# Optimization experiments

Measured on AMD Instinct MI355X. Metric: run time of the kernel, lower is better.

The kernel has to match this reference:

```python
import jax, jax.numpy as jnp
import numpy as np

N = 100000      # total nodes
E = 800000      # directed edges
DIN = 256       # input feature dim
H = 128         # hidden dim
EPS = 1e-5      # BatchNorm eps


def setup_inputs() -> dict:
    key = jax.random.key(0)
    ks = jax.random.split(key, 18)
    s = 0.05
    return {
        "x": jax.random.normal(ks[0], (N, DIN), jnp.float32),
        "src": jax.random.randint(ks[1], (E,), 0, N, dtype=jnp.int32),
        "dst": jax.random.randint(ks[2], (E,), 0, N, dtype=jnp.int32),
        "W1": jax.random.normal(ks[3], (DIN, H), jnp.float32) * s,
        "b1": jnp.zeros((H,), jnp.float32),
        "g1": jnp.ones((H,), jnp.float32),
        "be1": jnp.zeros((H,), jnp.float32),
        "W2": jax.random.normal(ks[4], (H, H), jnp.float32) * s,
        "b2": jnp.zeros((H,), jnp.float32),
        "g2": jnp.ones((H,), jnp.float32),
        "be2": jnp.zeros((H,), jnp.float32),
        "W3": jax.random.normal(ks[5], (H, H), jnp.float32) * s,
        "b3": jnp.zeros((H,), jnp.float32),
        "g3": jnp.ones((H,), jnp.float32),
        "be3": jnp.zeros((H,), jnp.float32),
        "Wf": jax.random.normal(ks[6], (H, 1), jnp.float32) * s,
        "bf": jnp.zeros((1,), jnp.float32),
    }


def _gcn_conv(h, W, b, src, dst, dis):
    # GCNConv: project, then sym-normalized aggregation over edges + self-loops
    h = h @ W                                   # [N, out]
    coef = dis[src] * dis[dst]                  # [E] edge norm weights
    agg = jax.ops.segment_sum(h[src] * coef[:, None], dst, num_segments=N)
    agg = agg + h * (dis * dis)[:, None]        # self-loop term (norm = 1/deg)
    return agg + b


def _bn_relu(h, g, be):
    # BatchNorm1d in training mode (batch stats over nodes, biased variance)
    mu = jnp.mean(h, axis=0)
    var = jnp.var(h, axis=0)
    return jax.nn.relu((h - mu) * (g / jnp.sqrt(var + EPS)) + be)


def reference(x, src, dst, W1, b1, g1, be1, W2, b2, g2, be2,
              W3, b3, g3, be3, Wf, bf):
    # degree of (A + I) counted on destination nodes, edge weight 1
    deg = jax.ops.segment_sum(jnp.ones((E,), jnp.float32), dst, num_segments=N) + 1.0
    dis = jax.lax.rsqrt(deg)                    # deg >= 1, safe

    h = _bn_relu(_gcn_conv(x, W1, b1, src, dst, dis), g1, be1)
    h = _bn_relu(_gcn_conv(h, W2, b2, src, dst, dis), g2, be2)
    h = _bn_relu(_gcn_conv(h, W3, b3, src, dst, dis), g3, be3)
    return h @ Wf + bf                          # [N, 1]
```

## Files before the change

### kernel.cpp

```cpp
#include <hip/hip_runtime.h>
#include <hip/hip_bf16.h>

typedef unsigned short ushort_t;
typedef __bf16 bf16x8 __attribute__((ext_vector_type(8)));
typedef unsigned short ushort8 __attribute__((ext_vector_type(8)));
typedef unsigned short ushort4v __attribute__((ext_vector_type(4)));
typedef float f32x4 __attribute__((ext_vector_type(4)));

#define HH 128
#define EPS 1e-5f
#define STAT_SLICES 32
#define MTILE 32
#define GAS __attribute__((address_space(1)))
#define LAS __attribute__((address_space(3)))

__device__ __forceinline__ float bf2f(ushort_t u) {
    unsigned v = ((unsigned)u) << 16;
    return __builtin_bit_cast(float, v);
}
__device__ __forceinline__ ushort_t f2bf(float f) {
    unsigned u = __builtin_bit_cast(unsigned, f);
    unsigned r = (u + 0x7fffu + ((u >> 16) & 1u)) >> 16;
    return (ushort_t)r;
}
__device__ __forceinline__ float cvt(const void* p, int i, int flag) {
    return flag ? bf2f(((const ushort_t*)p)[i]) : ((const float*)p)[i];
}
__device__ __forceinline__ void dma16(const void* g, void* l) {
    __builtin_amdgcn_global_load_lds((const GAS unsigned*)g, (LAS unsigned*)l, 16, 0, 0);
}
__device__ __forceinline__ void acc8(const uint4 w, float c, float a[8]) {
    unsigned x0 = w.x, x1 = w.y, x2 = w.z, x3 = w.w;
    a[0] = fmaf(__builtin_bit_cast(float, x0 << 16), c, a[0]);
    a[1] = fmaf(__builtin_bit_cast(float, x0 & 0xffff0000u), c, a[1]);
    a[2] = fmaf(__builtin_bit_cast(float, x1 << 16), c, a[2]);
    a[3] = fmaf(__builtin_bit_cast(float, x1 & 0xffff0000u), c, a[3]);
    a[4] = fmaf(__builtin_bit_cast(float, x2 << 16), c, a[4]);
    a[5] = fmaf(__builtin_bit_cast(float, x2 & 0xffff0000u), c, a[5]);
    a[6] = fmaf(__builtin_bit_cast(float, x3 << 16), c, a[6]);
    a[7] = fmaf(__builtin_bit_cast(float, x3 & 0xffff0000u), c, a[7]);
}

__global__ void preK(const int* __restrict__ dst, int* __restrict__ counts, int E,
                     const void* W1, ushort_t* Wt1, const void* W2, ushort_t* Wt2,
                     const void* W3, ushort_t* Wt3,
                     const void* g1, const void* b1, const void* b2, const void* b3,
                     const void* g2, const void* g3, const void* be1, const void* be2,
                     const void* be3, const void* Wfp, const void* bfp,
                     float* __restrict__ cvec, int histB) {
    const int bid = blockIdx.x;
    const int tid = threadIdx.x;
    const int flag = (((const ushort_t*)g1)[0] == 0x3F80) ? 1 : 0;
    if (bid < histB) {
        int e = bid * 256 + tid;
        if (e < E) atomicAdd(&counts[dst[e]], 1);
    } else if (bid < histB + 256) {
        int idx = (bid - histB) * 256 + tid;
        const void* W; ushort_t* Wt; int K;
        if (idx < 32768)      { W = W1; Wt = Wt1; K = 256; }
        else if (idx < 49152) { W = W2; Wt = Wt2; K = 128; idx -= 32768; }
        else                  { W = W3; Wt = Wt3; K = 128; idx -= 49152; }
        int k = idx >> 7, nn = idx & 127;
        Wt[nn * K + k] = flag ? ((const ushort_t*)W)[idx] : f2bf(((const float*)W)[idx]);
    } else {
        int t = tid;
        if (t < 128) {
            cvec[t]        = cvt(b1, t, flag);
            cvec[128 + t]  = cvt(b2, t, flag);
            cvec[256 + t]  = cvt(b3, t, flag);
            cvec[384 + t]  = cvt(g1, t, flag);
            cvec[512 + t]  = cvt(g2, t, flag);
            cvec[640 + t]  = cvt(g3, t, flag);
            cvec[768 + t]  = cvt(be1, t, flag);
            cvec[896 + t]  = cvt(be2, t, flag);
            cvec[1024 + t] = cvt(be3, t, flag);
            cvec[1152 + t] = cvt(Wfp, t, flag);
            if (t == 0) cvec[1280] = cvt(bfp, 0, flag);
        }
    }
}

__global__ void scanAdisK(const int* __restrict__ cnt, int* __restrict__ partial,
                          float* __restrict__ dis, int n, int nbScan) {
    __shared__ int lds[256];
    const int tid = threadIdx.x;
    if ((int)blockIdx.x < nbScan) {
        int base = blockIdx.x * 2048 + tid * 8;
        int s = 0;
#pragma unroll
        for (int j = 0; j < 8; ++j) { int idx = base + j; if (idx < n) s += cnt[idx]; }
        lds[tid] = s; __syncthreads();
        for (int off = 128; off; off >>= 1) { if (tid < off) lds[tid] += lds[tid + off]; __syncthreads(); }
        if (tid == 0) partial[blockIdx.x] = lds[0];
    } else {
        int i = (blockIdx.x - nbScan) * 256 + tid;
        if (i < n) dis[i] = rsqrtf((float)cnt[i] + 1.0f);
    }
}

__device__ __forceinline__ void scanC2Dev(int* lds, const int* __restrict__ cnt,
                                          const int* __restrict__ partial,
                                          int* __restrict__ rowptr, int n, int bid, int nb) {
    const int tid = threadIdx.x;
    int pre = 0, tot = 0;
    for (int i = 0; i < nb; ++i) { int v = partial[i]; if (i < bid) pre += v; tot += v; }
    int base = bid * 2048 + tid * 8;
    int v[8]; int s = 0;
#pragma unroll
    for (int j = 0; j < 8; ++j) { int idx = base + j; v[j] = (idx < n) ? cnt[idx] : 0; s += v[j]; }
    lds[tid] = s; __syncthreads();
    for (int off = 1; off < 256; off <<= 1) {
        int x = (tid >= off) ? lds[tid - off] : 0;
        __syncthreads();
        lds[tid] += x;
        __syncthreads();
    }
    int excl = lds[tid] - s;
    int off0 = pre + excl;
#pragma unroll
    for (int j = 0; j < 8; ++j) {
        int idx = base + j;
        if (idx < n) { rowptr[idx] = off0; off0 += v[j]; }
    }
    if (bid == 0 && tid == 0) rowptr[n] = tot;
}

__global__ void scatterK(const int* __restrict__ src, const int* __restrict__ dst,
                         const int* __restrict__ rowptr, int* __restrict__ fill,
                         const float* __restrict__ dis,
                         uint2* __restrict__ erec, int E) {
    int e = blockIdx.x * 256 + threadIdx.x;
    if (e >= E) return;
    int d = dst[e], s = src[e];
    int old = atomicSub(&fill[d], 1);
    int pos = rowptr[d] + old - 1;
    float c = dis[s] * dis[d];
    uint2 r; r.x = (unsigned)s; r.y = __builtin_bit_cast(unsigned, c);
    erec[pos] = r;
}

__global__ __launch_bounds__(256) void mm1scanCK(const void* __restrict__ x,
                                                 const ushort_t* __restrict__ Wt1,
                                                 ushort_t* __restrict__ tbuf, int n,
                                                 const ushort_t* __restrict__ flagRef,
                                                 const int* __restrict__ cnt,
                                                 const int* __restrict__ partial,
                                                 int* __restrict__ rowptr, int nbScan) {
    __shared__ char smem[33792];
    const int tid = threadIdx.x;
    if ((int)blockIdx.x < nbScan) {
        scanC2Dev((int*)smem, cnt, partial, rowptr, n, blockIdx.x, nbScan);
        return;
    }
    const int arm = blockIdx.x - nbScan;
    const int NB  = gridDim.x - nbScan;
    const int nTiles = (n + MTILE - 1) / MTILE;
    if (arm >= nTiles) return;

    const int lane = tid & 63, wave = tid >> 6;
    const int m = lane & 15, q = lane >> 4;
    const int flag = (flagRef[0] == 0x3F80) ? 1 : 0;

    ushort8 wfrag[8][2];
#pragma unroll
    for (int s = 0; s < 8; ++s)
#pragma unroll
        for (int tt = 0; tt < 2; ++tt)
            wfrag[s][tt] = *(const ushort8*)&Wt1[(size_t)((wave * 2 + tt) * 16 + m) * 256 + s * 32 + q * 8];

    const int sr = tid >> 3, sa = tid & 7;
    char* buf0 = smem;
    char* buf1 = smem + 16384;

    float4  f[8];
    ushort8 v[4];

    auto stageLoad = [&](int T) {
        int row = T * MTILE + sr; if (row >= n) row = n - 1;
        if (flag) {
            const ushort_t* xp = (const ushort_t*)x + (size_t)row * 256 + sa * 32;
#pragma unroll
            for (int j = 0; j < 4; ++j) v[j] = *(const ushort8*)(xp + j * 8);
        } else {
            const float* xp = (const float*)x + (size_t)row * 256 + sa * 32;
#pragma unroll
            for (int j = 0; j < 8; ++j) f[j] = *(const float4*)(xp + j * 4);
        }
    };
    auto convWrite = [&](char* buf) {
        if (!flag) {
#pragma unroll
            for (int j = 0; j < 4; ++j) {
                float4 a = f[2 * j], b = f[2 * j + 1];
                ushort8 t8;
                t8[0] = f2bf(a.x); t8[1] = f2bf(a.y); t8[2] = f2bf(a.z); t8[3] = f2bf(a.w);
                t8[4] = f2bf(b.x); t8[5] = f2bf(b.y); t8[6] = f2bf(b.z); t8[7] = f2bf(b.w);
                v[j] = t8;
            }
        }
#pragma unroll
        for (int j = 0; j < 4; ++j) {
            int u = (sa * 4 + j) ^ (sr & 7);
            *(ushort8*)(buf + sr * 512 + u * 16) = v[j];
        }
    };
    auto computeStore = [&](int T, const char* buf) {
        f32x4 acc[2][2];
#pragma unroll
        for (int bb = 0; bb < 2; ++bb)
#pragma unroll
            for (int tt = 0; tt < 2; ++tt) acc[bb][tt] = (f32x4){0.f, 0.f, 0.f, 0.f};
#pragma unroll
        for (int bb = 0; bb < 2; ++bb) {
            const char* base = buf + (bb * 16 + m) * 512;
#pragma unroll
            for (int s = 0; s < 8; ++s) {
                ushort8 xf = *(const ushort8*)(base + (((s * 4 + q) ^ (m & 7)) * 16));
                bf16x8 xb = __builtin_bit_cast(bf16x8, xf);
#pragma unroll
                for (int tt = 0; tt < 2; ++tt)
                    acc[bb][tt] = __builtin_amdgcn_mfma_f32_16x16x32_bf16(
                        __builtin_bit_cast(bf16x8, wfrag[s][tt]), xb, acc[bb][tt], 0, 0, 0);
            }
        }
#pragma unroll
        for (int bb = 0; bb < 2; ++bb) {
            int node = T * MTILE + bb * 16 + m;
            if (node < n) {
#pragma unroll
                for (int tt = 0; tt < 2; ++tt) {
                    ushort4v pk;
#pragma unroll
                    for (int r = 0; r < 4; ++r) pk[r] = f2bf(acc[bb][tt][r]);
                    *(ushort4v*)(tbuf + (size_t)node * HH + (wave * 2 + tt) * 16 + q * 4) = pk;
                }
            }
        }
    };

    stageLoad(arm); convWrite(buf0);
    __syncthreads();
    int T = arm, pp = 0;
    while (true) {
        int Tn = T + NB;
        bool more = (Tn < nTiles);
        if (more) stageLoad(Tn);
        computeStore(T, pp ? buf1 : buf0);
        if (!more) break;
        convWrite(pp ? buf0 : buf1);
        __syncthreads();
        T = Tn; pp ^= 1;
    }
}

__global__ __launch_bounds__(256) void mmBNK(const ushort_t* __restrict__ A,
                                             const ushort_t* __restrict__ Wt,
                                             ushort_t* __restrict__ out, int n,
                                             const float* __restrict__ ssum,
                                             const float* __restrict__ ssq,
                                             const float* __restrict__ gam,
                                             const float* __restrict__ bet) {
    __shared__ char smem[50176];
    char* abuf = smem + 32768;
    float* scw = (float*)(smem + 49152);
    const int tid = threadIdx.x;

    if (tid < 128) {
        float S = 0.f, Q = 0.f;
#pragma unroll
        for (int sl = 0; sl < STAT_SLICES; ++sl) { S += ssum[sl * HH + tid]; Q += ssq[sl * HH + tid]; }
        float invn = 1.0f / (float)n;
        float mu = S * invn;
        float var = fmaxf(Q * invn - mu * mu, 0.f);
        float sc = gam[tid] * rsqrtf(var + EPS);
        scw[tid] = sc;
        scw[128 + tid] = bet[tid] - mu * sc;
    }
#pragma unroll
    for (int it = 0; it < 8; ++it) {
        int idx = tid + it * 256;
        int r = idx >> 4, seg = idx & 15;
        int p = seg ^ (r & 7);
        *(uint4*)&smem[r * 256 + p * 16] = *(const uint4*)&Wt[(size_t)r * 128 + seg * 8];
    }
    __syncthreads();

    const int lane = tid & 63, wave = tid >> 6;
    const int m = lane & 15, q = lane >> 4;
    const int nTiles = (n + 63) >> 6;

    for (int tile = blockIdx.x; tile < nTiles; tile += gridDim.x) {
        const int row0 = tile * 64 + wave * 16;
#pragma unroll
        for (int j = 0; j < 4; ++j) {
            int r = row0 + j * 4;
            if (r + 3 >= n) r = n - 4;
            const char* g = (const char*)A + (size_t)r * 256 + lane * 16;
            dma16(g, abuf + (wave * 16 + j * 4) * 256);
        }
        __builtin_amdgcn_s_waitcnt(0x0F70);

        f32x4 acc[8];
#pragma unroll
        for (int t = 0; t < 8; ++t) acc[t] = (f32x4){0.f, 0.f, 0.f, 0.f};
        const char* arow = abuf + (wave * 16 + m) * 256;
#pragma unroll
        for (int s = 0; s < 4; ++s) {
            ushort8 av = *(const ushort8*)(arow + s * 64 + q * 16);
            int kb = s * 32 + q * 8;
#pragma unroll
            for (int j = 0; j < 8; ++j)
                av[j] = f2bf(fmaxf(bf2f(av[j]) * scw[kb + j] + scw[128 + kb + j], 0.f));
            bf16x8 nf = __builtin_bit_cast(bf16x8, av);
#pragma unroll
            for (int t = 0; t < 8; ++t) {
                int p = (s * 4 + q) ^ (m & 7);
                ushort8 wv = *(const ushort8*)&smem[(t * 16 + m) * 256 + p * 16];
                acc[t] = __builtin_amdgcn_mfma_f32_16x16x32_bf16(
                    __builtin_bit_cast(bf16x8, wv), nf, acc[t], 0, 0, 0);
            }
        }
        int node = tile * 64 + wave * 16 + m;
        if (node < n) {
            ushort_t* op = out + (size_t)node * HH + q * 4;
#pragma unroll
            for (int t = 0; t < 8; ++t) {
                ushort4v pk;
#pragma unroll
                for (int r = 0; r < 4; ++r) pk[r] = f2bf(acc[t][r]);
                *(ushort4v*)(op + t * 16) = pk;
            }
        }
    }
}

__global__ __launch_bounds__(256) void aggK(const ushort_t* __restrict__ t,
                                            const uint2* __restrict__ erec,
                                            const int* __restrict__ rowptr,
                                            const float* __restrict__ dis,
                                            const float* __restrict__ bias,
                                            ushort_t* __restrict__ g,
                                            float* __restrict__ ssum, float* __restrict__ ssq,
                                            int n) {
    const int tid  = threadIdx.x;
    const int lane = tid & 63;
    const int wave = tid >> 6;
    const int grp  = lane >> 4;
    const int p    = lane & 15;
    const int cb   = p * 8;

    float bch[8];
#pragma unroll
    for (int j = 0; j < 8; ++j) bch[j] = bias[cb + j];

    float s[8], q[8];
#pragma unroll
    for (int j = 0; j < 8; ++j) { s[j] = 0.f; q[j] = 0.f; }

    for (int node = blockIdx.x * 16 + wave * 4 + grp; node < n; node += gridDim.x * 16) {
        float d = dis[node];
        float d2 = d * d;
        float a[8];
#pragma unroll
        for (int j = 0; j < 8; ++j) a[j] = 0.f;
        uint4 sv = *(const uint4*)(t + (size_t)node * HH + cb);
        acc8(sv, d2, a);

        const int beg = rowptr[node], end = rowptr[node + 1];
        int e = beg;
        for (; e + 8 <= end; e += 8) {
            uint2 rr[8];
#pragma unroll
            for (int kk = 0; kk < 8; ++kk) rr[kk] = erec[e + kk];
            uint4 w0[4];
#pragma unroll
            for (int kk = 0; kk < 4; ++kk)
                w0[kk] = *(const uint4*)(t + (size_t)rr[kk].x * HH + cb);
            uint4 w1[4];
#pragma unroll
            for (int kk = 0; kk < 4; ++kk)
                w1[kk] = *(const uint4*)(t + (size_t)rr[4 + kk].x * HH + cb);
#pragma unroll
            for (int kk = 0; kk < 4; ++kk)
                acc8(w0[kk], __builtin_bit_cast(float, rr[kk].y), a);
#pragma unroll
            for (int kk = 0; kk < 4; ++kk)
                acc8(w1[kk], __builtin_bit_cast(float, rr[4 + kk].y), a);
        }
        if (e < end) {
            uint2 rr[8];
#pragma unroll
            for (int kk = 0; kk < 8; ++kk) {
                int idx = e + kk;
                rr[kk] = (idx < end) ? erec[idx] : (uint2){0u, 0u};
            }
            uint4 w0[4];
#pragma unroll
            for (int kk = 0; kk < 4; ++kk)
                w0[kk] = *(const uint4*)(t + (size_t)rr[kk].x * HH + cb);
            uint4 w1[4];
#pragma unroll
            for (int kk = 0; kk < 4; ++kk)
                w1[kk] = *(const uint4*)(t + (size_t)rr[4 + kk].x * HH + cb);
#pragma unroll
            for (int kk = 0; kk < 4; ++kk)
                acc8(w0[kk], __builtin_bit_cast(float, rr[kk].y), a);
#pragma unroll
            for (int kk = 0; kk < 4; ++kk)
                acc8(w1[kk], __builtin_bit_cast(float, rr[4 + kk].y), a);
        }

        ushort8 pk;
#pragma unroll
        for (int j = 0; j < 8; ++j) {
            a[j] += bch[j];
            pk[j] = f2bf(a[j]);
            s[j] += a[j]; q[j] += a[j] * a[j];
        }
        *(ushort8*)(g + (size_t)node * HH + cb) = pk;
    }

#pragma unroll
    for (int j = 0; j < 8; ++j) {
        s[j] += __shfl_xor(s[j], 16); s[j] += __shfl_xor(s[j], 32);
        q[j] += __shfl_xor(q[j], 16); q[j] += __shfl_xor(q[j], 32);
    }
    __shared__ float red[4][16][16];
    if (grp == 0) {
#pragma unroll
        for (int j = 0; j < 8; ++j) { red[wave][p][j] = s[j]; red[wave][p][8 + j] = q[j]; }
    }
    __syncthreads();
    {
        int ch = tid & 127, kind = tid >> 7;
        float S = 0.f;
#pragma unroll
        for (int w = 0; w < 4; ++w) S += red[w][ch >> 3][kind * 8 + (ch & 7)];
        int slice = (blockIdx.x & (STAT_SLICES - 1)) * HH;
        atomicAdd((kind ? ssq : ssum) + slice + ch, S);
    }
}

__global__ __launch_bounds__(256) void outK(const ushort_t* __restrict__ g,
                                            const float* __restrict__ ssum,
                                            const float* __restrict__ ssq,
                                            const float* __restrict__ gam,
                                            const float* __restrict__ bet,
                                            const float* __restrict__ Wf,
                                            const float* __restrict__ bfp,
                                            void* __restrict__ outv, int n,
                                            const ushort_t* __restrict__ flagRef) {
    __shared__ float scw[256];
    const int tid = threadIdx.x;
    if (tid < 128) {
        float S = 0.f, Q = 0.f;
#pragma unroll
        for (int sl = 0; sl < STAT_SLICES; ++sl) { S += ssum[sl * HH + tid]; Q += ssq[sl * HH + tid]; }
        float invn = 1.0f / (float)n;
        float mu = S * invn;
        float var = fmaxf(Q * invn - mu * mu, 0.f);
        float sc = gam[tid] * rsqrtf(var + EPS);
        scw[tid] = sc;
        scw[128 + tid] = bet[tid] - mu * sc;
    }
    __syncthreads();

    const int lane = tid & 63;
    const int wave = tid >> 6;
    const int grp  = lane >> 4;
    const int p    = lane & 15;
    const int cb   = p * 8;
    float w8[8], sc8[8], sh8[8];
#pragma unroll
    for (int j = 0; j < 8; ++j) {
        w8[j] = Wf[cb + j]; sc8[j] = scw[cb + j]; sh8[j] = scw[128 + cb + j];
    }
    const float bb = bfp[0];
    const int flag = (flagRef[0] == 0x3F80) ? 1 : 0;

    for (int node = blockIdx.x * 16 + wave * 4 + grp; node < n; node += gridDim.x * 16) {
        uint4 v = *(const uint4*)(g + (size_t)node * HH + cb);
        unsigned u[4] = {v.x, v.y, v.z, v.w};
        float x = 0.f;
#pragma unroll
        for (int j = 0; j < 4; ++j) {
            float f0 = __builtin_bit_cast(float, u[j] << 16);
            float f1 = __builtin_bit_cast(float, u[j] & 0xffff0000u);
            x += fmaxf(f0 * sc8[2 * j] + sh8[2 * j], 0.f) * w8[2 * j];
            x += fmaxf(f1 * sc8[2 * j + 1] + sh8[2 * j + 1], 0.f) * w8[2 * j + 1];
        }
#pragma unroll
        for (int off = 8; off; off >>= 1) x += __shfl_xor(x, off);
        if (p == 0) {
            float r = x + bb;
            if (flag) ((ushort_t*)outv)[node] = f2bf(r);
            else      ((float*)outv)[node] = r;
        }
    }
}

extern "C" void kernel_launch(void* const* d_in, const int* in_sizes, int n_in,
                              void* d_out, int out_size, void* d_ws, size_t ws_size,
                              hipStream_t stream) {
    const int DIN = 256;
    const int N = in_sizes[0] / DIN;
    const int E = in_sizes[1];

    const void* x   = d_in[0];
    const int*  src = (const int*)d_in[1];
    const int*  dst = (const int*)d_in[2];
    const void* W1  = d_in[3];
    const void* b1  = d_in[4];
    const void* g1  = d_in[5];
    const void* be1 = d_in[6];
    const void* W2  = d_in[7];
    const void* b2  = d_in[8];
    const void* g2  = d_in[9];
    const void* be2 = d_in[10];
    const void* W3  = d_in[11];
    const void* b3  = d_in[12];
    const void* g3  = d_in[13];
    const void* be3 = d_in[14];
    const void* Wf  = d_in[15];
    const void* bfp = d_in[16];
    const ushort_t* flagRef = (const ushort_t*)g1;

    char* base = (char*)d_ws;
    size_t off = 0;
    auto carve = [&](size_t bytes) -> void* {
        void* p = base + off;
        off += (bytes + 255) & ~(size_t)255;
        return p;
    };
    int*      counts = (int*)carve((size_t)N * 4);
    float*    stats  = (float*)carve((size_t)3 * 2 * STAT_SLICES * HH * 4);
    size_t    zbytes = off;
    float*    dis    = (float*)carve((size_t)N * 4);
    int*      rowptr = (int*)carve((size_t)(N + 1) * 4);
    int*      partial= (int*)carve(256 * 4);
    uint2*    erec   = (uint2*)carve((size_t)E * 8);
    ushort_t* Wt1    = (ushort_t*)carve((size_t)128 * 256 * 2);
    ushort_t* Wt2    = (ushort_t*)carve((size_t)128 * 128 * 2);
    ushort_t* Wt3    = (ushort_t*)carve((size_t)128 * 128 * 2);
    ushort_t* tbuf   = (ushort_t*)carve((size_t)N * HH * 2);
    ushort_t* gbuf   = (ushort_t*)carve((size_t)N * HH * 2);
    float*    cvec   = (float*)carve((size_t)1281 * 4);

    float* ssum0 = stats;                         float* ssq0 = ssum0 + STAT_SLICES * HH;
    float* ssum1 = ssq0 + STAT_SLICES * HH;       float* ssq1 = ssum1 + STAT_SLICES * HH;
    float* ssum2 = ssq1 + STAT_SLICES * HH;       float* ssq2 = ssum2 + STAT_SLICES * HH;

    float* c_b1 = cvec;         float* c_b2 = cvec + 128;  float* c_b3 = cvec + 256;
    float* c_g1 = cvec + 384;   float* c_g2 = cvec + 512;  float* c_g3 = cvec + 640;
    float* c_be1 = cvec + 768;  float* c_be2 = cvec + 896; float* c_be3 = cvec + 1024;
    float* c_Wf = cvec + 1152;  float* c_bf = cvec + 1280;

    const int nbScan = (N + 2047) / 2048;
    const int histB  = (E + 255) / 256;
    const int disB   = (N + 255) / 256;
    const int aggB   = 2048;
    const int mm1B   = 1024;

    hipMemsetAsync(d_ws, 0, zbytes, stream);

    preK<<<histB + 256 + 1, 256, 0, stream>>>(dst, counts, E, W1, Wt1, W2, Wt2, W3, Wt3,
                                              g1, b1, b2, b3, g2, g3, be1, be2, be3, Wf, bfp,
                                              cvec, histB);
    scanAdisK<<<nbScan + disB, 256, 0, stream>>>(counts, partial, dis, N, nbScan);
    mm1scanCK<<<nbScan + mm1B, 256, 0, stream>>>(x, Wt1, tbuf, N, flagRef,
                                                 counts, partial, rowptr, nbScan);
    scatterK<<<histB, 256, 0, stream>>>(src, dst, rowptr, counts, dis, erec, E);

    aggK<<<aggB, 256, 0, stream>>>(tbuf, erec, rowptr, dis, c_b1, gbuf, ssum0, ssq0, N);
    mmBNK<<<768, 256, 0, stream>>>(gbuf, Wt2, tbuf, N, ssum0, ssq0, c_g1, c_be1);
    aggK<<<aggB, 256, 0, stream>>>(tbuf, erec, rowptr, dis, c_b2, gbuf, ssum1, ssq1, N);
    mmBNK<<<768, 256, 0, stream>>>(gbuf, Wt3, tbuf, N, ssum1, ssq1, c_g2, c_be2);
    aggK<<<aggB, 256, 0, stream>>>(tbuf, erec, rowptr, dis, c_b3, gbuf, ssum2, ssq2, N);
    outK<<<1024, 256, 0, stream>>>(gbuf, ssum2, ssq2, c_g3, c_be3, c_Wf, c_bf, d_out, N, flagRef);
}
```

Before: 420.5 us.

## Fuse scatter, aggregation, matmul and output stages into one persistent kernel with grid barriers

Replaces the six kernel launches after the first matmul (scatter, three aggregations, two BN+matmul, output) with one persistent kernel of 1024 blocks that uses a software grid barrier (atomic counter plus release flag) between phases. The matmul phase is also restructured: weight fragments are held in registers, A tiles of 32 rows are double-buffered through LDS with swizzle, and the async LDS DMA path is dropped. This removes launch gaps and per-kernel ramp-up and tail costs. The risks are lower parallelism in the aggregation phases (1024 blocks instead of 2048), spin-wait cost at each barrier, and deadlock if the 1024 blocks cannot all be resident at once.

Result: slower. 1.182 ms (+181.0%).

```diff
diff --git a/kernel.cpp b/kernel.cpp
--- a/kernel.cpp
+++ b/kernel.cpp
@@ -11,8 +11,7 @@
 #define EPS 1e-5f
 #define STAT_SLICES 32
 #define MTILE 32
-#define GAS __attribute__((address_space(1)))
-#define LAS __attribute__((address_space(3)))
+#define FB 1024
 
 __device__ __forceinline__ float bf2f(ushort_t u) {
     unsigned v = ((unsigned)u) << 16;
@@ -25,9 +24,6 @@
 }
 __device__ __forceinline__ float cvt(const void* p, int i, int flag) {
     return flag ? bf2f(((const ushort_t*)p)[i]) : ((const float*)p)[i];
-}
-__device__ __forceinline__ void dma16(const void* g, void* l) {
-    __builtin_amdgcn_global_load_lds((const GAS unsigned*)g, (LAS unsigned*)l, 16, 0, 0);
 }
 __device__ __forceinline__ void acc8(const uint4 w, float c, float a[8]) {
     unsigned x0 = w.x, x1 = w.y, x2 = w.z, x3 = w.w;
@@ -39,6 +35,21 @@
     a[5] = fmaf(__builtin_bit_cast(float, x2 & 0xffff0000u), c, a[5]);
     a[6] = fmaf(__builtin_bit_cast(float, x3 << 16), c, a[6]);
     a[7] = fmaf(__builtin_bit_cast(float, x3 & 0xffff0000u), c, a[7]);
+}
+
+__device__ __forceinline__ void gridSync(int* cnt, int* rel, int phase, int nb) {
+    __syncthreads();
+    if (threadIdx.x == 0) {
+        __threadfence();
+        int prev = atomicAdd(cnt, 1);
+        if (prev == nb * phase - 1) {
+            atomicExch(rel, phase);
+        } else {
+            while (atomicAdd(rel, 0) < phase) __builtin_amdgcn_s_sleep(8);
+        }
+        __threadfence();
+    }
+    __syncthreads();
 }
 
 __global__ void preK(const int* __restrict__ dst, int* __restrict__ counts, int E,
@@ -125,20 +136,6 @@
     if (bid == 0 && tid == 0) rowptr[n] = tot;
 }
 
-__global__ void scatterK(const int* __restrict__ src, const int* __restrict__ dst,
-                         const int* __restrict__ rowptr, int* __restrict__ fill,
-                         const float* __restrict__ dis,
-                         uint2* __restrict__ erec, int E) {
-    int e = blockIdx.x * 256 + threadIdx.x;
-    if (e >= E) return;
-    int d = dst[e], s = src[e];
-    int old = atomicSub(&fill[d], 1);
-    int pos = rowptr[d] + old - 1;
-    float c = dis[s] * dis[d];
-    uint2 r; r.x = (unsigned)s; r.y = __builtin_bit_cast(unsigned, c);
-    erec[pos] = r;
-}
-
 __global__ __launch_bounds__(256) void mm1scanCK(const void* __restrict__ x,
                                                  const ushort_t* __restrict__ Wt1,
                                                  ushort_t* __restrict__ tbuf, int n,
@@ -253,248 +250,286 @@
     }
 }
 
-__global__ __launch_bounds__(256) void mmBNK(const ushort_t* __restrict__ A,
-                                             const ushort_t* __restrict__ Wt,
-                                             ushort_t* __restrict__ out, int n,
-                                             const float* __restrict__ ssum,
-                                             const float* __restrict__ ssq,
-                                             const float* __restrict__ gam,
-                                             const float* __restrict__ bet) {
-    __shared__ char smem[50176];
-    char* abuf = smem + 32768;
-    float* scw = (float*)(smem + 49152);
+__global__ __launch_bounds__(256, 4) void fusedK(
+        const int* __restrict__ src, const int* __restrict__ dst,
+        const int* __restrict__ rowptr, int* __restrict__ fill,
+        const float* __restrict__ dis, uint2* __restrict__ erec, int E,
+        const ushort_t* __restrict__ Wt2, const ushort_t* __restrict__ Wt3,
+        ushort_t* __restrict__ tbuf, ushort_t* __restrict__ gbuf,
+        const float* __restrict__ cvec, float* __restrict__ stats,
+        void* __restrict__ outv, int n, const ushort_t* __restrict__ flagRef,
+        int* __restrict__ bcnt, int* __restrict__ brel) {
+    __shared__ char smem[17408];
+    const int NB  = gridDim.x;
     const int tid = threadIdx.x;
-
-    if (tid < 128) {
-        float S = 0.f, Q = 0.f;
-#pragma unroll
-        for (int sl = 0; sl < STAT_SLICES; ++sl) { S += ssum[sl * HH + tid]; Q += ssq[sl * HH + tid]; }
-        float invn = 1.0f / (float)n;
-        float mu = S * invn;
-        float var = fmaxf(Q * invn - mu * mu, 0.f);
-        float sc = gam[tid] * rsqrtf(var + EPS);
-        scw[tid] = sc;
-        scw[128 + tid] = bet[tid] - mu * sc;
-    }
-#pragma unroll
-    for (int it = 0; it < 8; ++it) {
-        int idx = tid + it * 256;
-        int r = idx >> 4, seg = idx & 15;
-        int p = seg ^ (r & 7);
-        *(uint4*)&smem[r * 256 + p * 16] = *(const uint4*)&Wt[(size_t)r * 128 + seg * 8];
-    }
-    __syncthreads();
-
     const int lane = tid & 63, wave = tid >> 6;
-    const int m = lane & 15, q = lane >> 4;
-    const int nTiles = (n + 63) >> 6;
-
-    for (int tile = blockIdx.x; tile < nTiles; tile += gridDim.x) {
-        const int row0 = tile * 64 + wave * 16;
-#pragma unroll
-        for (int j = 0; j < 4; ++j) {
-            int r = row0 + j * 4;
-            if (r + 3 >= n) r = n - 4;
-            const char* g = (const char*)A + (size_t)r * 256 + lane * 16;
-            dma16(g, abuf + (wave * 16 + j * 4) * 256);
-        }
-        __builtin_amdgcn_s_waitcnt(0x0F70);
-
-        f32x4 acc[8];
-#pragma unroll
-        for (int t = 0; t < 8; ++t) acc[t] = (f32x4){0.f, 0.f, 0.f, 0.f};
-        const char* arow = abuf + (wave * 16 + m) * 256;
-#pragma unroll
-        for (int s = 0; s < 4; ++s) {
-            ushort8 av = *(const ushort8*)(arow + s * 64 + q * 16);
-            int kb = s * 32 + q * 8;
-#pragma unroll
-            for (int j = 0; j < 8; ++j)
-                av[j] = f2bf(fmaxf(bf2f(av[j]) * scw[kb + j] + scw[128 + kb + j], 0.f));
-            bf16x8 nf = __builtin_bit_cast(bf16x8, av);
-#pragma unroll
-            for (int t = 0; t < 8; ++t) {
-                int p = (s * 4 + q) ^ (m & 7);
-                ushort8 wv = *(const ushort8*)&smem[(t * 16 + m) * 256 + p * 16];
-                acc[t] = __builtin_amdgcn_mfma_f32_16x16x32_bf16(
-                    __builtin_bit_cast(bf16x8, wv), nf, acc[t], 0, 0, 0);
-            }
-        }
-        int node = tile * 64 + wave * 16 + m;
-        if (node < n) {
-            ushort_t* op = out + (size_t)node * HH + q * 4;
-#pragma unroll
-            for (int t = 0; t < 8; ++t) {
-                ushort4v pk;
-#pragma unroll
-                for (int r = 0; r < 4; ++r) pk[r] = f2bf(acc[t][r]);
-                *(ushort4v*)(op + t * 16) = pk;
-            }
-        }
-    }
-}
-
-__global__ __launch_bounds__(256) void aggK(const ushort_t* __restrict__ t,
-                                            const uint2* __restrict__ erec,
-                                            const int* __restrict__ rowptr,
-                                            const float* __restrict__ dis,
-                                            const float* __restrict__ bias,
-                                            ushort_t* __restrict__ g,
-                                            float* __restrict__ ssum, float* __restrict__ ssq,
-                                            int n) {
-    const int tid  = threadIdx.x;
-    const int lane = tid & 63;
-    const int wave = tid >> 6;
-    const int grp  = lane >> 4;
-    const int p    = lane & 15;
-    const int cb   = p * 8;
-
-    float bch[8];
-#pragma unroll
-    for (int j = 0; j < 8; ++j) bch[j] = bias[cb + j];
-
-    float s[8], q[8];
-#pragma unroll
-    for (int j = 0; j < 8; ++j) { s[j] = 0.f; q[j] = 0.f; }
-
-    for (int node = blockIdx.x * 16 + wave * 4 + grp; node < n; node += gridDim.x * 16) {
-        float d = dis[node];
-        float d2 = d * d;
-        float a[8];
-#pragma unroll
-        for (int j = 0; j < 8; ++j) a[j] = 0.f;
-        uint4 sv = *(const uint4*)(t + (size_t)node * HH + cb);
-        acc8(sv, d2, a);
-
-        const int beg = rowptr[node], end = rowptr[node + 1];
-        int e = beg;
-        for (; e + 8 <= end; e += 8) {
-            uint2 rr[8];
-#pragma unroll
-            for (int kk = 0; kk < 8; ++kk) rr[kk] = erec[e + kk];
-            uint4 w0[4];
-#pragma unroll
-            for (int kk = 0; kk < 4; ++kk)
-                w0[kk] = *(const uint4*)(t + (size_t)rr[kk].x * HH + cb);
-            uint4 w1[4];
-#pragma unroll
-            for (int kk = 0; kk < 4; ++kk)
-                w1[kk] = *(const uint4*)(t + (size_t)rr[4 + kk].x * HH + cb);
-#pragma unroll
-            for (int kk = 0; kk < 4; ++kk)
-                acc8(w0[kk], __builtin_bit_cast(float, rr[kk].y), a);
-#pragma unroll
-            for (int kk = 0; kk < 4; ++kk)
-                acc8(w1[kk], __builtin_bit_cast(float, rr[4 + kk].y), a);
-        }
-        if (e < end) {
-            uint2 rr[8];
-#pragma unroll
-            for (int kk = 0; kk < 8; ++kk) {
-                int idx = e + kk;
-                rr[kk] = (idx < end) ? erec[idx] : (uint2){0u, 0u};
-            }
-            uint4 w0[4];
-#pragma unroll
-            for (int kk = 0; kk < 4; ++kk)
-                w0[kk] = *(const uint4*)(t + (size_t)rr[kk].x * HH + cb);
-            uint4 w1[4];
-#pragma unroll
-            for (int kk = 0; kk < 4; ++kk)
-                w1[kk] = *(const uint4*)(t + (size_t)rr[4 + kk].x * HH + cb);
-#pragma unroll
-            for (int kk = 0; kk < 4; ++kk)
-                acc8(w0[kk], __builtin_bit_cast(float, rr[kk].y), a);
-#pragma unroll
-            for (int kk = 0; kk < 4; ++kk)
-                acc8(w1[kk], __builtin_bit_cast(float, rr[4 + kk].y), a);
-        }
-
-        ushort8 pk;
+
+    const float* c_b1  = cvec;        const float* c_b2  = cvec + 128;
+    const float* c_b3  = cvec + 256;  const float* c_g1  = cvec + 384;
+    const float* c_g2  = cvec + 512;  const float* c_g3  = cvec + 640;
+    const float* c_be1 = cvec + 768;  const float* c_be2 = cvec + 896;
+    const float* c_be3 = cvec + 1024; const float* c_Wf  = cvec + 1152;
+    const float* c_bf  = cvec + 1280;
+    float* ssum0 = stats;            float* ssq0 = stats + 4096;
+    float* ssum1 = stats + 8192;     float* ssq1 = stats + 12288;
+    float* ssum2 = stats + 16384;    float* ssq2 = stats + 20480;
+
+    for (int e = blockIdx.x * 256 + tid; e < E; e += NB * 256) {
+        int d = dst[e], s = src[e];
+        int old = atomicSub(&fill[d], 1);
+        int pos = rowptr[d] + old - 1;
+        float c = dis[s] * dis[d];
+        uint2 r; r.x = (unsigned)s; r.y = __builtin_bit_cast(unsigned, c);
+        erec[pos] = r;
+    }
+
+    auto aggPhase = [&](const ushort_t* __restrict__ t, ushort_t* __restrict__ g,
+                        const float* __restrict__ bias,
+                        float* __restrict__ ssum, float* __restrict__ ssq) {
+        const int grp = lane >> 4, p = lane & 15, cb = p * 8;
+        float bch[8];
+#pragma unroll
+        for (int j = 0; j < 8; ++j) bch[j] = bias[cb + j];
+        float s[8], q[8];
+#pragma unroll
+        for (int j = 0; j < 8; ++j) { s[j] = 0.f; q[j] = 0.f; }
+
+        for (int node = blockIdx.x * 16 + wave * 4 + grp; node < n; node += NB * 16) {
+            float d = dis[node];
+            float d2 = d * d;
+            float a[8];
+#pragma unroll
+            for (int j = 0; j < 8; ++j) a[j] = 0.f;
+            uint4 sv = *(const uint4*)(t + (size_t)node * HH + cb);
+            acc8(sv, d2, a);
+
+            const int beg = rowptr[node], end = rowptr[node + 1];
+            int e = beg;
+            for (; e + 8 <= end; e += 8) {
+                uint2 rr[8];
+#pragma unroll
+                for (int kk = 0; kk < 8; ++kk) rr[kk] = erec[e + kk];
+                uint4 w0[4];
+#pragma unroll
+                for (int kk = 0; kk < 4; ++kk)
+                    w0[kk] = *(const uint4*)(t + (size_t)rr[kk].x * HH + cb);
+                uint4 w1[4];
+#pragma unroll
+                for (int kk = 0; kk < 4; ++kk)
+                    w1[kk] = *(const uint4*)(t + (size_t)rr[4 + kk].x * HH + cb);
+#pragma unroll
+                for (int kk = 0; kk < 4; ++kk)
+                    acc8(w0[kk], __builtin_bit_cast(float, rr[kk].y), a);
+#pragma unroll
+                for (int kk = 0; kk < 4; ++kk)
+                    acc8(w1[kk], __builtin_bit_cast(float, rr[4 + kk].y), a);
+            }
+            if (e < end) {
+                uint2 rr[8];
+#pragma unroll
+                for (int kk = 0; kk < 8; ++kk) {
+                    int idx = e + kk;
+                    rr[kk] = (idx < end) ? erec[idx] : (uint2){0u, 0u};
+                }
+                uint4 w0[4];
+#pragma unroll
+                for (int kk = 0; kk < 4; ++kk)
+                    w0[kk] = *(const uint4*)(t + (size_t)rr[kk].x * HH + cb);
+                uint4 w1[4];
+#pragma unroll
+                for (int kk = 0; kk < 4; ++kk)
+                    w1[kk] = *(const uint4*)(t + (size_t)rr[4 + kk].x * HH + cb);
+#pragma unroll
+                for (int kk = 0; kk < 4; ++kk)
+                    acc8(w0[kk], __builtin_bit_cast(float, rr[kk].y), a);
+#pragma unroll
+                for (int kk = 0; kk < 4; ++kk)
+                    acc8(w1[kk], __builtin_bit_cast(float, rr[4 + kk].y), a);
+            }
+
+            ushort8 pk;
+#pragma unroll
+            for (int j = 0; j < 8; ++j) {
+                a[j] += bch[j];
+                pk[j] = f2bf(a[j]);
+                s[j] += a[j]; q[j] += a[j] * a[j];
+            }
+            *(ushort8*)(g + (size_t)node * HH + cb) = pk;
+        }
+
 #pragma unroll
         for (int j = 0; j < 8; ++j) {
-            a[j] += bch[j];
-            pk[j] = f2bf(a[j]);
-            s[j] += a[j]; q[j] += a[j] * a[j];
-        }
-        *(ushort8*)(g + (size_t)node * HH + cb) = pk;
-    }
-
-#pragma unroll
-    for (int j = 0; j < 8; ++j) {
-        s[j] += __shfl_xor(s[j], 16); s[j] += __shfl_xor(s[j], 32);
-        q[j] += __shfl_xor(q[j], 16); q[j] += __shfl_xor(q[j], 32);
-    }
-    __shared__ float red[4][16][16];
-    if (grp == 0) {
-#pragma unroll
-        for (int j = 0; j < 8; ++j) { red[wave][p][j] = s[j]; red[wave][p][8 + j] = q[j]; }
-    }
-    __syncthreads();
+            s[j] += __shfl_xor(s[j], 16); s[j] += __shfl_xor(s[j], 32);
+            q[j] += __shfl_xor(q[j], 16); q[j] += __shfl_xor(q[j], 32);
+        }
+        float (*red)[16][16] = (float (*)[16][16])smem;
+        __syncthreads();
+        if (grp == 0) {
+#pragma unroll
+            for (int j = 0; j < 8; ++j) { red[wave][p][j] = s[j]; red[wave][p][8 + j] = q[j]; }
+        }
+        __syncthreads();
+        {
+            int ch = tid & 127, kind = tid >> 7;
+            float S = 0.f;
+#pragma unroll
+            for (int w = 0; w < 4; ++w) S += red[w][ch >> 3][kind * 8 + (ch & 7)];
+            int slice = (blockIdx.x & (STAT_SLICES - 1)) * HH;
+            atomicAdd((kind ? ssq : ssum) + slice + ch, S);
+        }
+    };
+
+    auto mmPhase = [&](const ushort_t* __restrict__ A, const ushort_t* __restrict__ Wt,
+                       ushort_t* __restrict__ out,
+                       const float* __restrict__ ssum, const float* __restrict__ ssq,
+                       const float* __restrict__ gam, const float* __restrict__ bet) {
+        float* scw = (float*)(smem + 16384);
+        if (tid < 128) {
+            float S = 0.f, Q = 0.f;
+#pragma unroll
+            for (int sl = 0; sl < STAT_SLICES; ++sl) { S += ssum[sl * HH + tid]; Q += ssq[sl * HH + tid]; }
+            float invn = 1.0f / (float)n;
+            float mu = S * invn;
+            float var = fmaxf(Q * invn - mu * mu, 0.f);
+            float sc = gam[tid] * rsqrtf(var + EPS);
+            scw[tid] = sc;
+            scw[128 + tid] = bet[tid] - mu * sc;
+        }
+        const int m = lane & 15, q4 = lane >> 4;
+        ushort8 wfrag[4][2];
+#pragma unroll
+        for (int s = 0; s < 4; ++s)
+#pragma unroll
+            for (int tt = 0; tt < 2; ++tt)
+                wfrag[s][tt] = *(const ushort8*)&Wt[(size_t)((wave * 2 + tt) * 16 + m) * 128 + s * 32 + q4 * 8];
+
+        const int sr = tid >> 3, sa = tid & 7;
+        char* b0 = smem;
+        char* b1 = smem + 8192;
+        ushort8 sv[2];
+
+        auto sLoad = [&](int T) {
+            int row = T * 32 + sr; if (row >= n) row = n - 1;
+            const ushort_t* ap = A + (size_t)row * HH + sa * 16;
+            sv[0] = *(const ushort8*)ap;
+            sv[1] = *(const ushort8*)(ap + 8);
+        };
+        auto sWrite = [&](char* buf) {
+#pragma unroll
+            for (int j = 0; j < 2; ++j) {
+                int u = (sa * 2 + j) ^ (sr & 7);
+                *(ushort8*)(buf + sr * 256 + u * 16) = sv[j];
+            }
+        };
+        auto comp = [&](int T, const char* buf) {
+            f32x4 acc[2][2];
+#pragma unroll
+            for (int bb = 0; bb < 2; ++bb)
+#pragma unroll
+                for (int tt = 0; tt < 2; ++tt) acc[bb][tt] = (f32x4){0.f, 0.f, 0.f, 0.f};
+#pragma unroll
+            for (int bb = 0; bb < 2; ++bb) {
+                const char* arow = buf + (bb * 16 + m) * 256;
+#pragma unroll
+                for (int s = 0; s < 4; ++s) {
+                    ushort8 av = *(const ushort8*)(arow + (((s * 4 + q4) ^ (m & 7)) * 16));
+                    int kb = s * 32 + q4 * 8;
+#pragma unroll
+                    for (int j = 0; j < 8; ++j)
+                        av[j] = f2bf(fmaxf(bf2f(av[j]) * scw[kb + j] + scw[128 + kb + j], 0.f));
+                    bf16x8 nf = __builtin_bit_cast(bf16x8, av);
+#pragma unroll
+                    for (int tt = 0; tt < 2; ++tt)
+                        acc[bb][tt] = __builtin_amdgcn_mfma_f32_16x16x32_bf16(
+                            __builtin_bit_cast(bf16x8, wfrag[s][tt]), nf, acc[bb][tt], 0, 0, 0);
+                }
+            }
+#pragma unroll
+            for (int bb = 0; bb < 2; ++bb) {
+                int node = T * 32 + bb * 16 + m;
+                if (node < n) {
+#pragma unroll
+                    for (int tt = 0; tt < 2; ++tt) {
+                        ushort4v pk;
+#pragma unroll
+                        for (int r = 0; r < 4; ++r) pk[r] = f2bf(acc[bb][tt][r]);
+                        *(ushort4v*)(out + (size_t)node * HH + (wave * 2 + tt) * 16 + q4 * 4) = pk;
+                    }
+                }
+            }
+        };
+
+        const int nT = (n + 31) >> 5;
+        int T = blockIdx.x, pp = 0;
+        if (T < nT) sLoad(T);
+        __syncthreads();
+        if (T < nT) sWrite(b0);
+        __syncthreads();
+        while (T < nT) {
+            int Tn = T + NB;
+            if (Tn < nT) sLoad(Tn);
+            comp(T, pp ? b1 : b0);
+            if (Tn >= nT) break;
+            sWrite(pp ? b0 : b1);
+            __syncthreads();
+            T = Tn; pp ^= 1;
+        }
+    };
+
+    gridSync(bcnt, brel, 1, NB);
+    aggPhase(tbuf, gbuf, c_b1, ssum0, ssq0);
+    gridSync(bcnt, brel, 2, NB);
+    mmPhase(gbuf, Wt2, tbuf, ssum0, ssq0, c_g1, c_be1);
+    gridSync(bcnt, brel, 3, NB);
+    aggPhase(tbuf, gbuf, c_b2, ssum1, ssq1);
+    gridSync(bcnt, brel, 4, NB);
+    mmPhase(gbuf, Wt3, tbuf, ssum1, ssq1, c_g2, c_be2);
+    gridSync(bcnt, brel, 5, NB);
+    aggPhase(tbuf, gbuf, c_b3, ssum2, ssq2);
+    gridSync(bcnt, brel, 6, NB);
+
     {
-        int ch = tid & 127, kind = tid >> 7;
-        float S = 0.f;
-#pragma unroll
-        for (int w = 0; w < 4; ++w) S += red[w][ch >> 3][kind * 8 + (ch & 7)];
-        int slice = (blockIdx.x & (STAT_SLICES - 1)) * HH;
-        atomicAdd((kind ? ssq : ssum) + slice + ch, S);
-    }
-}
-
-__global__ __launch_bounds__(256) void outK(const ushort_t* __restrict__ g,
-                                            const float* __restrict__ ssum,
-                                            const float* __restrict__ ssq,
-                                            const float* __restrict__ gam,
-                                            const float* __restrict__ bet,
-                                            const float* __restrict__ Wf,
-                                            const float* __restrict__ bfp,
-                                            void* __restrict__ outv, int n,
-                                            const ushort_t* __restrict__ flagRef) {
-    __shared__ float scw[256];
-    const int tid = threadIdx.x;
-    if (tid < 128) {
-        float S = 0.f, Q = 0.f;
-#pragma unroll
-        for (int sl = 0; sl < STAT_SLICES; ++sl) { S += ssum[sl * HH + tid]; Q += ssq[sl * HH + tid]; }
-        float invn = 1.0f / (float)n;
-        float mu = S * invn;
-        float var = fmaxf(Q * invn - mu * mu, 0.f);
-        float sc = gam[tid] * rsqrtf(var + EPS);
-        scw[tid] = sc;
-        scw[128 + tid] = bet[tid] - mu * sc;
-    }
-    __syncthreads();
-
-    const int lane = tid & 63;
-    const int wave = tid >> 6;
-    const int grp  = lane >> 4;
-    const int p    = lane & 15;
-    const int cb   = p * 8;
-    float w8[8], sc8[8], sh8[8];
-#pragma unroll
-    for (int j = 0; j < 8; ++j) {
-        w8[j] = Wf[cb + j]; sc8[j] = scw[cb + j]; sh8[j] = scw[128 + cb + j];
-    }
-    const float bb = bfp[0];
-    const int flag = (flagRef[0] == 0x3F80) ? 1 : 0;
-
-    for (int node = blockIdx.x * 16 + wave * 4 + grp; node < n; node += gridDim.x * 16) {
-        uint4 v = *(const uint4*)(g + (size_t)node * HH + cb);
-        unsigned u[4] = {v.x, v.y, v.z, v.w};
-        float x = 0.f;
-#pragma unroll
-        for (int j = 0; j < 4; ++j) {
-            float f0 = __builtin_bit_cast(float, u[j] << 16);
-            float f1 = __builtin_bit_cast(float, u[j] & 0xffff0000u);
-            x += fmaxf(f0 * sc8[2 * j] + sh8[2 * j], 0.f) * w8[2 * j];
-            x += fmaxf(f1 * sc8[2 * j + 1] + sh8[2 * j + 1], 0.f) * w8[2 * j + 1];
-        }
-#pragma unroll
-        for (int off = 8; off; off >>= 1) x += __shfl_xor(x, off);
-        if (p == 0) {
-            float r = x + bb;
-            if (flag) ((ushort_t*)outv)[node] = f2bf(r);
-            else      ((float*)outv)[node] = r;
+        float* scw = (float*)(smem + 16384);
+        if (tid < 128) {
+            float S = 0.f, Q = 0.f;
+#pragma unroll
+            for (int sl = 0; sl < STAT_SLICES; ++sl) { S += ssum2[sl * HH + tid]; Q += ssq2[sl * HH + tid]; }
+            float invn = 1.0f / (float)n;
+            float mu = S * invn;
+            float var = fmaxf(Q * invn - mu * mu, 0.f);
+            float sc = c_g3[tid] * rsqrtf(var + EPS);
+            scw[tid] = sc;
+            scw[128 + tid] = c_be3[tid] - mu * sc;
+        }
+        __syncthreads();
+
+        const int grp = lane >> 4, p = lane & 15, cb = p * 8;
+        float w8[8], sc8[8], sh8[8];
+#pragma unroll
+        for (int j = 0; j < 8; ++j) {
+            w8[j] = c_Wf[cb + j]; sc8[j] = scw[cb + j]; sh8[j] = scw[128 + cb + j];
+        }
+        const float bb = c_bf[0];
+        const int flag = (flagRef[0] == 0x3F80) ? 1 : 0;
+
+        for (int node = blockIdx.x * 16 + wave * 4 + grp; node < n; node += NB * 16) {
+            uint4 v = *(const uint4*)(gbuf + (size_t)node * HH + cb);
+            unsigned u[4] = {v.x, v.y, v.z, v.w};
+            float x = 0.f;
+#pragma unroll
+            for (int j = 0; j < 4; ++j) {
+                float f0 = __builtin_bit_cast(float, u[j] << 16);
+                float f1 = __builtin_bit_cast(float, u[j] & 0xffff0000u);
+                x += fmaxf(f0 * sc8[2 * j] + sh8[2 * j], 0.f) * w8[2 * j];
+                x += fmaxf(f1 * sc8[2 * j + 1] + sh8[2 * j + 1], 0.f) * w8[2 * j + 1];
+            }
+#pragma unroll
+            for (int off = 8; off; off >>= 1) x += __shfl_xor(x, off);
+            if (p == 0) {
+                float r = x + bb;
+                if (flag) ((ushort_t*)outv)[node] = f2bf(r);
+                else      ((float*)outv)[node] = r;
+            }
         }
     }
 }
@@ -534,6 +569,7 @@
     };
     int*      counts = (int*)carve((size_t)N * 4);
     float*    stats  = (float*)carve((size_t)3 * 2 * STAT_SLICES * HH * 4);
+    int*      bar    = (int*)carve(256);
     size_t    zbytes = off;
     float*    dis    = (float*)carve((size_t)N * 4);
     int*      rowptr = (int*)carve((size_t)(N + 1) * 4);
@@ -546,19 +582,9 @@
     ushort_t* gbuf   = (ushort_t*)carve((size_t)N * HH * 2);
     float*    cvec   = (float*)carve((size_t)1281 * 4);
 
-    float* ssum0 = stats;                         float* ssq0 = ssum0 + STAT_SLICES * HH;
-    float* ssum1 = ssq0 + STAT_SLICES * HH;       float* ssq1 = ssum1 + STAT_SLICES * HH;
-    float* ssum2 = ssq1 + STAT_SLICES * HH;       float* ssq2 = ssum2 + STAT_SLICES * HH;
-
-    float* c_b1 = cvec;         float* c_b2 = cvec + 128;  float* c_b3 = cvec + 256;
-    float* c_g1 = cvec + 384;   float* c_g2 = cvec + 512;  float* c_g3 = cvec + 640;
-    float* c_be1 = cvec + 768;  float* c_be2 = cvec + 896; float* c_be3 = cvec + 1024;
-    float* c_Wf = cvec + 1152;  float* c_bf = cvec + 1280;
-
     const int nbScan = (N + 2047) / 2048;
     const int histB  = (E + 255) / 256;
     const int disB   = (N + 255) / 256;
-    const int aggB   = 2048;
     const int mm1B   = 1024;
 
     hipMemsetAsync(d_ws, 0, zbytes, stream);
@@ -569,12 +595,7 @@
     scanAdisK<<<nbScan + disB, 256, 0, stream>>>(counts, partial, dis, N, nbScan);
     mm1scanCK<<<nbScan + mm1B, 256, 0, stream>>>(x, Wt1, tbuf, N, flagRef,
                                                  counts, partial, rowptr, nbScan);
-    scatterK<<<histB, 256, 0, stream>>>(src, dst, rowptr, counts, dis, erec, E);
-
-    aggK<<<aggB, 256, 0, stream>>>(tbuf, erec, rowptr, dis, c_b1, gbuf, ssum0, ssq0, N);
-    mmBNK<<<768, 256, 0, stream>>>(gbuf, Wt2, tbuf, N, ssum0, ssq0, c_g1, c_be1);
-    aggK<<<aggB, 256, 0, stream>>>(tbuf, erec, rowptr, dis, c_b2, gbuf, ssum1, ssq1, N);
-    mmBNK<<<768, 256, 0, stream>>>(gbuf, Wt3, tbuf, N, ssum1, ssq1, c_g2, c_be2);
-    aggK<<<aggB, 256, 0, stream>>>(tbuf, erec, rowptr, dis, c_b3, gbuf, ssum2, ssq2, N);
-    outK<<<1024, 256, 0, stream>>>(gbuf, ssum2, ssq2, c_g3, c_be3, c_Wf, c_bf, d_out, N, flagRef);
-}
+    fusedK<<<FB, 256, 0, stream>>>(src, dst, rowptr, counts, dis, erec, E,
+                                   Wt2, Wt3, tbuf, gbuf, cvec, stats,
+                                   d_out, N, flagRef, &bar[0], &bar[1]);
+}
```
